# Kernel tuning notes

Hardware: AMD Instinct MI355X
Metric: run time of the kernel (lower is better)

The kernel has to match this reference:

```python
import jax, jax.numpy as jnp
import numpy as np

NUM_CATEGORIES = 10
FEATURE_DIM = 256
TEMPERATURE = 0.07
BATCH = 131072


def _l2norm(x, axis=-1, eps=1e-12):
    # matches torch F.normalize: x / max(||x||, eps)
    n = jnp.sqrt(jnp.sum(x * x, axis=axis, keepdims=True))
    return x / jnp.maximum(n, eps)


def setup_inputs() -> dict:
    key = jax.random.key(0)
    k1, k2, k3 = jax.random.split(key, 3)
    features = jax.random.normal(k1, (BATCH, FEATURE_DIM), dtype=jnp.float32)
    category_ids = jax.random.randint(k2, (BATCH,), 0, NUM_CATEGORIES, dtype=jnp.int32)
    # learned prototypes parameter, row-normalized at init as in the module
    prototypes = _l2norm(jax.random.normal(k3, (NUM_CATEGORIES, FEATURE_DIM), dtype=jnp.float32), axis=1)
    return {"features": features, "category_ids": category_ids, "prototypes": prototypes}


def reference(features, category_ids, prototypes):
    f = _l2norm(features, axis=1)  # [B, D]

    # per-category masked mean (segment mean), EMA prototype update (no_grad in torch)
    sums = jax.ops.segment_sum(f, category_ids, num_segments=NUM_CATEGORIES)  # [C, D]
    counts = jax.ops.segment_sum(jnp.ones((f.shape[0],), f.dtype), category_ids,
                                 num_segments=NUM_CATEGORIES)  # [C]
    means = sums / jnp.maximum(counts, 1.0)[:, None]
    ema = _l2norm(0.9 * prototypes + 0.1 * means, axis=1)
    updated = jnp.where((counts > 0)[:, None], ema, prototypes)  # [C, D]
    # torch writes into prototypes.data: value changes, param stays the autograd leaf
    p_used = prototypes + jax.lax.stop_gradient(updated - prototypes)

    # contrastive loss: one-hot cross entropy over categories
    sim = (f @ p_used.T) / TEMPERATURE  # [B, C]
    logp = jax.nn.log_softmax(sim, axis=1)
    b = f.shape[0]
    loss = -jnp.mean(logp[jnp.arange(b), category_ids])

    # align each feature with its category prototype
    aligned = _l2norm(0.7 * f + 0.3 * p_used[category_ids], axis=1)  # [B, D]
    return (loss, aligned)
```

## Files before the change

### kernel.cpp

```cpp
#include <hip/hip_runtime.h>

#define B_TOTAL 131072
#define DIM 256
#define NCAT 10

#define K1_BLOCKS 1024
#define K1_WAVES  (K1_BLOCKS * 4)
#define K3_BLOCKS 1024
#define NPART 16
#define SLABS_PER_PART (K1_BLOCKS / NPART)

#define SCR_STRIDE 2576
#define WS_SCRATCH 0
#define WS_PART2   (K1_BLOCKS * SCR_STRIDE)
#define WS_PUSED   (WS_PART2 + NCAT * NPART * 272)
#define WS_K3PART  (WS_PUSED + NCAT * DIM)

typedef __attribute__((ext_vector_type(8))) short bf16x8;
typedef __attribute__((ext_vector_type(4))) float f32x4;

union Frag { bf16x8 v; unsigned u[4]; };

__device__ __forceinline__ float waveRedSum(float v) {
#pragma unroll
  for (int m = 1; m < 64; m <<= 1) v += __shfl_xor(v, m, 64);
  return v;
}

__device__ __forceinline__ unsigned pk2(float a, float b) {
  unsigned ua = __float_as_uint(a), ub = __float_as_uint(b);
  ua = (ua + 0x7fffu + ((ua >> 16) & 1u)) >> 16;
  ub = (ub + 0x7fffu + ((ub >> 16) & 1u)) >> 16;
  return ua | (ub << 16);
}

__global__ __launch_bounds__(256) void k1_segsum(
    const float* __restrict__ feats, const int* __restrict__ cats,
    float* __restrict__ scratch) {
  __shared__ float acc[4][NCAT * DIM];
  __shared__ float accCnt[4][16];

  const int tid = threadIdx.x;
  const int w = tid >> 6;
  const int lane = tid & 63;

  for (int i = tid; i < 4 * NCAT * DIM; i += 256) (&acc[0][0])[i] = 0.0f;
  __syncthreads();

  float* accW = acc[w];
  int cnt = 0;
  int qd = blockIdx.x * 4 + w;

  const float* fp = feats + (size_t)qd * 4 * DIM + lane * 4;
  float4 A0 = *(const float4*)(fp);
  float4 A1 = *(const float4*)(fp + DIM);
  float4 A2 = *(const float4*)(fp + 2 * DIM);
  float4 A3 = *(const float4*)(fp + 3 * DIM);
  int c0 = cats[4 * qd], c1 = cats[4 * qd + 1];
  int c2 = cats[4 * qd + 2], c3 = cats[4 * qd + 3];

  for (int it = 0; it < 8; ++it) {
    const int qn = qd + K1_WAVES;
    float4 B0, B1, B2, B3;
    int d0 = 0, d1 = 0, d2 = 0, d3 = 0;
    if (it < 7) {
      const float* fn = feats + (size_t)qn * 4 * DIM + lane * 4;
      B0 = *(const float4*)(fn);
      B1 = *(const float4*)(fn + DIM);
      B2 = *(const float4*)(fn + 2 * DIM);
      B3 = *(const float4*)(fn + 3 * DIM);
      d0 = cats[4 * qn]; d1 = cats[4 * qn + 1];
      d2 = cats[4 * qn + 2]; d3 = cats[4 * qn + 3];
    }

    float s0 = A0.x * A0.x + A0.y * A0.y + A0.z * A0.z + A0.w * A0.w;
    float s1 = A1.x * A1.x + A1.y * A1.y + A1.z * A1.z + A1.w * A1.w;
    float s2 = A2.x * A2.x + A2.y * A2.y + A2.z * A2.z + A2.w * A2.w;
    float s3 = A3.x * A3.x + A3.y * A3.y + A3.z * A3.z + A3.w * A3.w;
#pragma unroll
    for (int m = 1; m < 64; m <<= 1) {
      s0 += __shfl_xor(s0, m, 64);
      s1 += __shfl_xor(s1, m, 64);
      s2 += __shfl_xor(s2, m, 64);
      s3 += __shfl_xor(s3, m, 64);
    }
    const float i0 = __builtin_amdgcn_rsqf(fmaxf(s0, 1e-24f));
    const float i1 = __builtin_amdgcn_rsqf(fmaxf(s1, 1e-24f));
    const float i2 = __builtin_amdgcn_rsqf(fmaxf(s2, 1e-24f));
    const float i3 = __builtin_amdgcn_rsqf(fmaxf(s3, 1e-24f));

    float4* p;
    float4 t;
    p = (float4*)&accW[c0 * DIM + lane * 4]; t = *p;
    t.x += A0.x * i0; t.y += A0.y * i0; t.z += A0.z * i0; t.w += A0.w * i0; *p = t;
    p = (float4*)&accW[c1 * DIM + lane * 4]; t = *p;
    t.x += A1.x * i1; t.y += A1.y * i1; t.z += A1.z * i1; t.w += A1.w * i1; *p = t;
    p = (float4*)&accW[c2 * DIM + lane * 4]; t = *p;
    t.x += A2.x * i2; t.y += A2.y * i2; t.z += A2.z * i2; t.w += A2.w * i2; *p = t;
    p = (float4*)&accW[c3 * DIM + lane * 4]; t = *p;
    t.x += A3.x * i3; t.y += A3.y * i3; t.z += A3.z * i3; t.w += A3.w * i3; *p = t;

    cnt += (lane == c0) + (lane == c1) + (lane == c2) + (lane == c3);

    if (it < 7) {
      A0 = B0; A1 = B1; A2 = B2; A3 = B3;
      c0 = d0; c1 = d1; c2 = d2; c3 = d3;
      qd = qn;
    }
  }

  if (lane < 16) accCnt[w][lane] = (float)cnt;
  __syncthreads();

  float* dst = scratch + (size_t)blockIdx.x * SCR_STRIDE;
  for (int i = tid; i < NCAT * DIM; i += 256)
    dst[i] = acc[0][i] + acc[1][i] + acc[2][i] + acc[3][i];
  if (tid < 16)
    dst[2560 + tid] = accCnt[0][tid] + accCnt[1][tid]
                    + accCnt[2][tid] + accCnt[3][tid];
}

__global__ __launch_bounds__(256) void k2a_reduce(
    const float* __restrict__ scratch, float* __restrict__ part) {
  const int b = blockIdx.x;
  const int c = b >> 4, p = b & 15;
  const int d = threadIdx.x;

  const float* base = scratch + (size_t)p * SLABS_PER_PART * SCR_STRIDE + c * DIM + d;
  float s0 = 0.f, s1 = 0.f, s2 = 0.f, s3 = 0.f;
#pragma unroll 4
  for (int s = 0; s < SLABS_PER_PART; s += 4) {
    s0 += base[(size_t)s * SCR_STRIDE];
    s1 += base[(size_t)(s + 1) * SCR_STRIDE];
    s2 += base[(size_t)(s + 2) * SCR_STRIDE];
    s3 += base[(size_t)(s + 3) * SCR_STRIDE];
  }
  part[b * 272 + d] = (s0 + s1) + (s2 + s3);

  if (d < 64) {
    float cn = scratch[((size_t)p * SLABS_PER_PART + d) * SCR_STRIDE + 2560 + c];
    cn = waveRedSum(cn);
    if (d == 0) part[b * 272 + 256] = cn;
  }
}

__global__ __launch_bounds__(256) void k2b_ema(
    const float* __restrict__ protos, const float* __restrict__ part,
    float* __restrict__ pused) {
  __shared__ float red[4];
  const int c = blockIdx.x;
  const int d = threadIdx.x;
  const int w = d >> 6, lane = d & 63;

  float s = 0.f, cnt = 0.f;
#pragma unroll
  for (int p = 0; p < NPART; p++) {
    s += part[(c * NPART + p) * 272 + d];
    cnt += part[(c * NPART + p) * 272 + 256];
  }

  const float pv = protos[c * DIM + d];
  const float v = 0.9f * pv + 0.1f * (s / fmaxf(cnt, 1.0f));

  float vv = waveRedSum(v * v);
  if (lane == 0) red[w] = vv;
  __syncthreads();
  const float n = fmaxf(sqrtf(red[0] + red[1] + red[2] + red[3]), 1e-12f);

  pused[c * DIM + d] = (cnt > 0.0f) ? v / n : pv;
}

__global__ __launch_bounds__(256) void k3_main(
    const float* __restrict__ feats, const int* __restrict__ cats,
    const float* __restrict__ pused, float* __restrict__ out,
    float* __restrict__ partials) {
  __shared__ unsigned short ot[4][16 * 272];
  __shared__ float wloss[4];

  const int tid = threadIdx.x;
  const int w = tid >> 6;
  const int l = tid & 63;
  const int q = l >> 4;
  const int mr = l & 15;
  char* otb = (char*)&ot[w][0];

  Frag bfr[8];
  {
    const float* prow = pused + mr * DIM;
#pragma unroll
    for (int s = 0; s < 8; s++) {
      float4 b0 = make_float4(0.f, 0.f, 0.f, 0.f), b1 = b0;
      const int kb = q * 8 + 32 * s;
      if (mr < NCAT) {
        b0 = *(const float4*)(prow + kb);
        b1 = *(const float4*)(prow + kb + 4);
      }
      bfr[s].u[0] = pk2(b0.x, b0.y); bfr[s].u[1] = pk2(b0.z, b0.w);
      bfr[s].u[2] = pk2(b1.x, b1.y); bfr[s].u[3] = pk2(b1.z, b1.w);
    }
  }

  constexpr float KZ = (1.0f / 0.07f) * 1.44269504088896f;
  constexpr float LN2 = 0.69314718056f;
  float lossAcc = 0.0f;

  const int waveG = blockIdx.x * 4 + w;
  const int nwaves = K3_BLOCKS * 4;

  for (int t = waveG; t < B_TOTAL / 16; t += nwaves) {
    const int r0 = t * 16;

    const float* frow = feats + (size_t)(r0 + mr) * DIM;
    Frag afr[8];
    float ss = 0.0f;
#pragma unroll
    for (int s = 0; s < 8; s++) {
      const int kb = q * 8 + 32 * s;
      const float4 u0 = *(const float4*)(frow + kb);
      const float4 u1 = *(const float4*)(frow + kb + 4);
      ss += u0.x * u0.x + u0.y * u0.y + u0.z * u0.z + u0.w * u0.w
          + u1.x * u1.x + u1.y * u1.y + u1.z * u1.z + u1.w * u1.w;
      afr[s].u[0] = pk2(u0.x, u0.y); afr[s].u[1] = pk2(u0.z, u0.w);
      afr[s].u[2] = pk2(u1.x, u1.y); afr[s].u[3] = pk2(u1.z, u1.w);
    }
    ss += __shfl_xor(ss, 16, 64);
    ss += __shfl_xor(ss, 32, 64);
    const float inv = __builtin_amdgcn_rsqf(fmaxf(ss, 1e-24f));

    f32x4 acc = {0.f, 0.f, 0.f, 0.f};
#pragma unroll
    for (int s = 0; s < 8; s++)
      acc = __builtin_amdgcn_mfma_f32_16x16x32_bf16(afr[s].v, bfr[s].v, acc, 0, 0, 0);

    float stv[4];
#pragma unroll
    for (int j = 0; j < 4; j++) {
      const float invj = __shfl(inv, 4 * q + j, 64);
      const int catj = cats[r0 + 4 * q + j];
      const float z = acc[j] * (invj * KZ);
      float zm = (mr < NCAT) ? z : -3.0e38f;
#pragma unroll
      for (int m = 1; m < 16; m <<= 1) zm = fmaxf(zm, __shfl_xor(zm, m, 64));
      float e = (mr < NCAT) ? __builtin_amdgcn_exp2f(z - zm) : 0.0f;
      float sv = (mr == catj) ? z : 0.0f;
#pragma unroll
      for (int m = 1; m < 16; m <<= 1) {
        e += __shfl_xor(e, m, 64);
        sv += __shfl_xor(sv, m, 64);
      }
      lossAcc += LN2 * (zm + __builtin_amdgcn_logf(e) - sv);
      stv[j] = sv;
    }

    const int srcg = (mr >> 2) * 16;
    const float s0 = __shfl(stv[0], srcg, 64);
    const float s1 = __shfl(stv[1], srcg, 64);
    const float s2 = __shfl(stv[2], srcg, 64);
    const float s3 = __shfl(stv[3], srcg, 64);
    const int jj = mr & 3;
    const float stm = (jj == 0) ? s0 : ((jj == 1) ? s1 : ((jj == 2) ? s2 : s3));
    const float simn = stm * (0.07f * LN2);
    const float inv2 = __builtin_amdgcn_rsqf(fmaxf(0.58f + 0.42f * simn, 1e-24f));
    const int catm = cats[r0 + mr];
    const float c0 = 0.7f * inv;
    const int psrc = q * 16 + catm;
    const int wrb = mr * 544;
    const int wsz = (mr & 7) << 4;

#pragma unroll
    for (int s = 0; s < 8; s++) {
      const int kb = q * 8 + 32 * s;
      unsigned pw0 = __shfl((int)bfr[s].u[0], psrc, 64);
      unsigned pw1 = __shfl((int)bfr[s].u[1], psrc, 64);
      unsigned pw2 = __shfl((int)bfr[s].u[2], psrc, 64);
      unsigned pw3 = __shfl((int)bfr[s].u[3], psrc, 64);
      const unsigned pws[4] = {pw0, pw1, pw2, pw3};
      float av[8];
#pragma unroll
      for (int h = 0; h < 4; h++) {
        const unsigned fp = afr[s].u[h];
        const unsigned pp = pws[h];
        const float f0 = __uint_as_float(fp << 16);
        const float f1 = __uint_as_float(fp & 0xffff0000u);
        const float p0 = __uint_as_float(pp << 16);
        const float p1 = __uint_as_float(pp & 0xffff0000u);
        av[2 * h]     = (c0 * f0 + 0.3f * p0) * inv2;
        av[2 * h + 1] = (c0 * f1 + 0.3f * p1) * inv2;
      }
      uint4 pk;
      pk.x = pk2(av[0], av[1]); pk.y = pk2(av[2], av[3]);
      pk.z = pk2(av[4], av[5]); pk.w = pk2(av[6], av[7]);
      *(uint4*)(otb + ((wrb + 2 * kb) ^ wsz)) = pk;
    }

    float* outr = out + (size_t)r0 * DIM;
#pragma unroll
    for (int i = 0; i < 16; ++i) {
      if (i == 15 && l == 63) continue;
      const int kidx = i * 64 + l + 1;
      const int rb = 544 * i;
      const int sz = (i & 7) << 4;
      const int cb = 8 * l + 6;
      float v[4];
#pragma unroll
      for (int c = 0; c < 4; ++c) {
        int a = (rb + cb + 2 * c) ^ sz;
        if (c > 0 && l == 63)
          a = (544 * (i + 1) + 2 * (c - 1)) ^ (((i + 1) & 7) << 4);
        v[c] = __uint_as_float((unsigned)(*(const unsigned short*)(otb + a)) << 16);
      }
      f32x4 sv = {v[0], v[1], v[2], v[3]};
      __builtin_nontemporal_store(sv, (f32x4*)(outr + 4 * kidx));
    }
    if (l < 3) {
      const float ev = __uint_as_float(
          (unsigned)(*(const unsigned short*)(otb + 2 * l)) << 16);
      __builtin_nontemporal_store(ev, outr + 1 + l);
    }
    if (l == 3) {
      const float ev = __uint_as_float(
          (unsigned)(*(const unsigned short*)(otb + ((544 * 15 + 510) ^ 112))) << 16);
      __builtin_nontemporal_store(ev, outr + 4096);
    }
  }

  const float s = waveRedSum(lossAcc);
  if (l == 0) wloss[w] = s * 0.0625f;
  __syncthreads();
  if (tid == 0)
    partials[blockIdx.x] = wloss[0] + wloss[1] + wloss[2] + wloss[3];
}

__global__ __launch_bounds__(256) void k4_loss(
    const float* __restrict__ partials, float* __restrict__ out) {
  __shared__ float red[4];
  const int tid = threadIdx.x;
  const int w = tid >> 6;
  const int lane = tid & 63;
  float s = 0.0f;
  for (int i = tid; i < K3_BLOCKS; i += 256) s += partials[i];
  s = waveRedSum(s);
  if (lane == 0) red[w] = s;
  __syncthreads();
  if (tid == 0)
    out[0] = (red[0] + red[1] + red[2] + red[3]) * (1.0f / (float)B_TOTAL);
}

extern "C" void kernel_launch(void* const* d_in, const int* in_sizes, int n_in,
                              void* d_out, int out_size, void* d_ws, size_t ws_size,
                              hipStream_t stream) {
  const float* feats = (const float*)d_in[0];
  const int* cats = (const int*)d_in[1];
  const float* protos = (const float*)d_in[2];
  float* out = (float*)d_out;
  float* ws = (float*)d_ws;

  k1_segsum<<<K1_BLOCKS, 256, 0, stream>>>(feats, cats, ws + WS_SCRATCH);
  k2a_reduce<<<NCAT * NPART, 256, 0, stream>>>(ws + WS_SCRATCH, ws + WS_PART2);
  k2b_ema<<<NCAT, 256, 0, stream>>>(protos, ws + WS_PART2, ws + WS_PUSED);
  k3_main<<<K3_BLOCKS, 256, 0, stream>>>(feats, cats, ws + WS_PUSED, out, ws + WS_K3PART);
  k4_loss<<<1, 256, 0, stream>>>(ws + WS_K3PART, out);
}
```

Before: 89.11 us.

## Cache normalized bf16 features from segsum pass and reuse in main kernel

The first kernel now writes the L2-normalized features as packed bf16 to workspace (64 MB fp32 read becomes a 32 MB bf16 write there). The main kernel then reads this half-size buffer instead of re-reading fp32 features and recomputing norms. The first kernel's feature loads are also made nontemporal. Net traffic changes from two 128 MB fp32 reads to one fp32 read plus a 64 MB bf16 write and a 64 MB bf16 read, and it adds 64 MB of workspace.

```diff
diff --git a/kernel.cpp b/kernel.cpp
--- a/kernel.cpp
+++ b/kernel.cpp
@@ -10,14 +10,16 @@
 #define NPART 16
 #define SLABS_PER_PART (K1_BLOCKS / NPART)
 
+#define WS_FHAT    0
+#define WS_SCRATCH (B_TOTAL * (DIM / 2))
 #define SCR_STRIDE 2576
-#define WS_SCRATCH 0
-#define WS_PART2   (K1_BLOCKS * SCR_STRIDE)
+#define WS_PART2   (WS_SCRATCH + K1_BLOCKS * SCR_STRIDE)
 #define WS_PUSED   (WS_PART2 + NCAT * NPART * 272)
 #define WS_K3PART  (WS_PUSED + NCAT * DIM)
 
 typedef __attribute__((ext_vector_type(8))) short bf16x8;
 typedef __attribute__((ext_vector_type(4))) float f32x4;
+typedef __attribute__((ext_vector_type(2))) unsigned u32x2;
 
 union Frag { bf16x8 v; unsigned u[4]; };
 
@@ -36,7 +38,7 @@
 
 __global__ __launch_bounds__(256) void k1_segsum(
     const float* __restrict__ feats, const int* __restrict__ cats,
-    float* __restrict__ scratch) {
+    unsigned* __restrict__ fhat, float* __restrict__ scratch) {
   __shared__ float acc[4][NCAT * DIM];
   __shared__ float accCnt[4][16];
 
@@ -51,24 +53,23 @@
   int cnt = 0;
   int qd = blockIdx.x * 4 + w;
 
-  const float* fp = feats + (size_t)qd * 4 * DIM + lane * 4;
-  float4 A0 = *(const float4*)(fp);
-  float4 A1 = *(const float4*)(fp + DIM);
-  float4 A2 = *(const float4*)(fp + 2 * DIM);
-  float4 A3 = *(const float4*)(fp + 3 * DIM);
+  const f32x4* fb = (const f32x4*)feats;
+  f32x4 A0 = __builtin_nontemporal_load(fb + (size_t)(4 * qd)     * 64 + lane);
+  f32x4 A1 = __builtin_nontemporal_load(fb + (size_t)(4 * qd + 1) * 64 + lane);
+  f32x4 A2 = __builtin_nontemporal_load(fb + (size_t)(4 * qd + 2) * 64 + lane);
+  f32x4 A3 = __builtin_nontemporal_load(fb + (size_t)(4 * qd + 3) * 64 + lane);
   int c0 = cats[4 * qd], c1 = cats[4 * qd + 1];
   int c2 = cats[4 * qd + 2], c3 = cats[4 * qd + 3];
 
   for (int it = 0; it < 8; ++it) {
     const int qn = qd + K1_WAVES;
-    float4 B0, B1, B2, B3;
+    f32x4 B0, B1, B2, B3;
     int d0 = 0, d1 = 0, d2 = 0, d3 = 0;
     if (it < 7) {
-      const float* fn = feats + (size_t)qn * 4 * DIM + lane * 4;
-      B0 = *(const float4*)(fn);
-      B1 = *(const float4*)(fn + DIM);
-      B2 = *(const float4*)(fn + 2 * DIM);
-      B3 = *(const float4*)(fn + 3 * DIM);
+      B0 = __builtin_nontemporal_load(fb + (size_t)(4 * qn)     * 64 + lane);
+      B1 = __builtin_nontemporal_load(fb + (size_t)(4 * qn + 1) * 64 + lane);
+      B2 = __builtin_nontemporal_load(fb + (size_t)(4 * qn + 2) * 64 + lane);
+      B3 = __builtin_nontemporal_load(fb + (size_t)(4 * qn + 3) * 64 + lane);
       d0 = cats[4 * qn]; d1 = cats[4 * qn + 1];
       d2 = cats[4 * qn + 2]; d3 = cats[4 * qn + 3];
     }
@@ -88,6 +89,16 @@
     const float i1 = __builtin_amdgcn_rsqf(fmaxf(s1, 1e-24f));
     const float i2 = __builtin_amdgcn_rsqf(fmaxf(s2, 1e-24f));
     const float i3 = __builtin_amdgcn_rsqf(fmaxf(s3, 1e-24f));
+
+    u32x2 h;
+    h.x = pk2(A0.x * i0, A0.y * i0); h.y = pk2(A0.z * i0, A0.w * i0);
+    *(u32x2*)(fhat + (size_t)(4 * qd)     * 128 + lane * 2) = h;
+    h.x = pk2(A1.x * i1, A1.y * i1); h.y = pk2(A1.z * i1, A1.w * i1);
+    *(u32x2*)(fhat + (size_t)(4 * qd + 1) * 128 + lane * 2) = h;
+    h.x = pk2(A2.x * i2, A2.y * i2); h.y = pk2(A2.z * i2, A2.w * i2);
+    *(u32x2*)(fhat + (size_t)(4 * qd + 2) * 128 + lane * 2) = h;
+    h.x = pk2(A3.x * i3, A3.y * i3); h.y = pk2(A3.z * i3, A3.w * i3);
+    *(u32x2*)(fhat + (size_t)(4 * qd + 3) * 128 + lane * 2) = h;
 
     float4* p;
     float4 t;
@@ -171,7 +182,7 @@
 }
 
 __global__ __launch_bounds__(256) void k3_main(
-    const float* __restrict__ feats, const int* __restrict__ cats,
+    const unsigned* __restrict__ fhat, const int* __restrict__ cats,
     const float* __restrict__ pused, float* __restrict__ out,
     float* __restrict__ partials) {
   __shared__ unsigned short ot[4][16 * 272];
@@ -210,22 +221,14 @@
   for (int t = waveG; t < B_TOTAL / 16; t += nwaves) {
     const int r0 = t * 16;
 
-    const float* frow = feats + (size_t)(r0 + mr) * DIM;
+    const uint4* fr = (const uint4*)(fhat + (size_t)(r0 + mr) * 128);
     Frag afr[8];
-    float ss = 0.0f;
 #pragma unroll
     for (int s = 0; s < 8; s++) {
-      const int kb = q * 8 + 32 * s;
-      const float4 u0 = *(const float4*)(frow + kb);
-      const float4 u1 = *(const float4*)(frow + kb + 4);
-      ss += u0.x * u0.x + u0.y * u0.y + u0.z * u0.z + u0.w * u0.w
-          + u1.x * u1.x + u1.y * u1.y + u1.z * u1.z + u1.w * u1.w;
-      afr[s].u[0] = pk2(u0.x, u0.y); afr[s].u[1] = pk2(u0.z, u0.w);
-      afr[s].u[2] = pk2(u1.x, u1.y); afr[s].u[3] = pk2(u1.z, u1.w);
-    }
-    ss += __shfl_xor(ss, 16, 64);
-    ss += __shfl_xor(ss, 32, 64);
-    const float inv = __builtin_amdgcn_rsqf(fmaxf(ss, 1e-24f));
+      const uint4 tt = fr[q + 4 * s];
+      afr[s].u[0] = tt.x; afr[s].u[1] = tt.y;
+      afr[s].u[2] = tt.z; afr[s].u[3] = tt.w;
+    }
 
     f32x4 acc = {0.f, 0.f, 0.f, 0.f};
 #pragma unroll
@@ -235,9 +238,8 @@
     float stv[4];
 #pragma unroll
     for (int j = 0; j < 4; j++) {
-      const float invj = __shfl(inv, 4 * q + j, 64);
       const int catj = cats[r0 + 4 * q + j];
-      const float z = acc[j] * (invj * KZ);
+      const float z = acc[j] * KZ;
       float zm = (mr < NCAT) ? z : -3.0e38f;
 #pragma unroll
       for (int m = 1; m < 16; m <<= 1) zm = fmaxf(zm, __shfl_xor(zm, m, 64));
@@ -262,7 +264,6 @@
     const float simn = stm * (0.07f * LN2);
     const float inv2 = __builtin_amdgcn_rsqf(fmaxf(0.58f + 0.42f * simn, 1e-24f));
     const int catm = cats[r0 + mr];
-    const float c0 = 0.7f * inv;
     const int psrc = q * 16 + catm;
     const int wrb = mr * 544;
     const int wsz = (mr & 7) << 4;
@@ -284,8 +285,8 @@
         const float f1 = __uint_as_float(fp & 0xffff0000u);
         const float p0 = __uint_as_float(pp << 16);
         const float p1 = __uint_as_float(pp & 0xffff0000u);
-        av[2 * h]     = (c0 * f0 + 0.3f * p0) * inv2;
-        av[2 * h + 1] = (c0 * f1 + 0.3f * p1) * inv2;
+        av[2 * h]     = (0.7f * f0 + 0.3f * p0) * inv2;
+        av[2 * h + 1] = (0.7f * f1 + 0.3f * p1) * inv2;
       }
       uint4 pk;
       pk.x = pk2(av[0], av[1]); pk.y = pk2(av[2], av[3]);
@@ -354,10 +355,11 @@
   const float* protos = (const float*)d_in[2];
   float* out = (float*)d_out;
   float* ws = (float*)d_ws;
-
-  k1_segsum<<<K1_BLOCKS, 256, 0, stream>>>(feats, cats, ws + WS_SCRATCH);
+  unsigned* fhat = (unsigned*)d_ws;
+
+  k1_segsum<<<K1_BLOCKS, 256, 0, stream>>>(feats, cats, fhat, ws + WS_SCRATCH);
   k2a_reduce<<<NCAT * NPART, 256, 0, stream>>>(ws + WS_SCRATCH, ws + WS_PART2);
   k2b_ema<<<NCAT, 256, 0, stream>>>(protos, ws + WS_PART2, ws + WS_PUSED);
-  k3_main<<<K3_BLOCKS, 256, 0, stream>>>(feats, cats, ws + WS_PUSED, out, ws + WS_K3PART);
+  k3_main<<<K3_BLOCKS, 256, 0, stream>>>(fhat, cats, ws + WS_PUSED, out, ws + WS_K3PART);
   k4_loss<<<1, 256, 0, stream>>>(ws + WS_K3PART, out);
 }
```

New measurement: 92.11 us. 1.03x slower.

## Fuse all stages into one cooperative kernel with bf16 normalized-feature cache

Applied to the files above, without the earlier changes.

Replaces the five-kernel chain with a single cooperative kernel of 512 blocks that uses grid.sync between the segment-sum, partial-reduce, EMA, main loss/align, and final-reduce phases. The first phase writes L2-normalized features as bf16 to workspace, so the main phase reads half the bytes and skips recomputing norms. Counts are now recomputed from category ids in the reduce phase. The change removes launch gaps and the second fp32 feature read, at the cost of grid-wide barriers, an extra bf16 write plus read of the features, and reduced parallelism. It falls back to the old multi-kernel path if cooperative launch is unavailable.

```diff
diff --git a/kernel.cpp b/kernel.cpp
--- a/kernel.cpp
+++ b/kernel.cpp
@@ -1,23 +1,16 @@
 #include <hip/hip_runtime.h>
+#include <hip/hip_cooperative_groups.h>
+
+namespace cg = cooperative_groups;
 
 #define B_TOTAL 131072
 #define DIM 256
 #define NCAT 10
-
-#define K1_BLOCKS 1024
-#define K1_WAVES  (K1_BLOCKS * 4)
-#define K3_BLOCKS 1024
 #define NPART 16
-#define SLABS_PER_PART (K1_BLOCKS / NPART)
-
-#define SCR_STRIDE 2576
-#define WS_SCRATCH 0
-#define WS_PART2   (K1_BLOCKS * SCR_STRIDE)
-#define WS_PUSED   (WS_PART2 + NCAT * NPART * 272)
-#define WS_K3PART  (WS_PUSED + NCAT * DIM)
 
 typedef __attribute__((ext_vector_type(8))) short bf16x8;
 typedef __attribute__((ext_vector_type(4))) float f32x4;
+typedef __attribute__((ext_vector_type(2))) unsigned u32x2;
 
 union Frag { bf16x8 v; unsigned u[4]; };
 
@@ -34,7 +27,329 @@
   return ua | (ub << 16);
 }
 
-__global__ __launch_bounds__(256) void k1_segsum(
+#define C_NB 512
+#define C_NWAVES (C_NB * 4)
+#define C_NQ (B_TOTAL / 4)
+#define C_SPP (C_NB / NPART)
+
+#define C_FHAT   0
+#define C_SCR    (B_TOTAL * (DIM / 2))
+#define C_PART   (C_SCR + C_NB * 2560)
+#define C_PUSED  (C_PART + NCAT * NPART * 272)
+#define C_LOSSP  (C_PUSED + NCAT * DIM)
+
+__global__ __launch_bounds__(256, 2) void kfused(
+    const float* __restrict__ feats, const int* __restrict__ cats,
+    const float* __restrict__ protos, float* __restrict__ out,
+    float* ws) {
+  __shared__ union {
+    float acc[4][NCAT * DIM];
+    struct { unsigned short ot[4][16 * 272]; float wloss[4]; } d;
+    float red[8];
+  } lds;
+
+  unsigned* fhat = (unsigned*)ws;
+  float* scratch = ws + C_SCR;
+  float* part = ws + C_PART;
+  float* pused = ws + C_PUSED;
+  float* lossp = ws + C_LOSSP;
+
+  const int tid = threadIdx.x;
+  const int blk = blockIdx.x;
+  const int w = tid >> 6;
+  const int lane = tid & 63;
+  cg::grid_group grid = cg::this_grid();
+
+  for (int i = tid; i < 4 * NCAT * DIM; i += 256) (&lds.acc[0][0])[i] = 0.0f;
+  __syncthreads();
+  {
+    float* accW = lds.acc[w];
+    const f32x4* fb = (const f32x4*)feats;
+    int qd = blk * 4 + w;
+
+    f32x4 A0 = fb[(size_t)(4 * qd)     * 64 + lane];
+    f32x4 A1 = fb[(size_t)(4 * qd + 1) * 64 + lane];
+    f32x4 A2 = fb[(size_t)(4 * qd + 2) * 64 + lane];
+    f32x4 A3 = fb[(size_t)(4 * qd + 3) * 64 + lane];
+    int c0 = cats[4 * qd], c1 = cats[4 * qd + 1];
+    int c2 = cats[4 * qd + 2], c3 = cats[4 * qd + 3];
+
+    for (;;) {
+      const int qn = qd + C_NWAVES;
+      const bool more = qn < C_NQ;
+      f32x4 B0, B1, B2, B3;
+      int d0 = 0, d1 = 0, d2 = 0, d3 = 0;
+      if (more) {
+        B0 = fb[(size_t)(4 * qn)     * 64 + lane];
+        B1 = fb[(size_t)(4 * qn + 1) * 64 + lane];
+        B2 = fb[(size_t)(4 * qn + 2) * 64 + lane];
+        B3 = fb[(size_t)(4 * qn + 3) * 64 + lane];
+        d0 = cats[4 * qn]; d1 = cats[4 * qn + 1];
+        d2 = cats[4 * qn + 2]; d3 = cats[4 * qn + 3];
+      }
+
+      float s0 = A0.x * A0.x + A0.y * A0.y + A0.z * A0.z + A0.w * A0.w;
+      float s1 = A1.x * A1.x + A1.y * A1.y + A1.z * A1.z + A1.w * A1.w;
+      float s2 = A2.x * A2.x + A2.y * A2.y + A2.z * A2.z + A2.w * A2.w;
+      float s3 = A3.x * A3.x + A3.y * A3.y + A3.z * A3.z + A3.w * A3.w;
+#pragma unroll
+      for (int m = 1; m < 64; m <<= 1) {
+        s0 += __shfl_xor(s0, m, 64);
+        s1 += __shfl_xor(s1, m, 64);
+        s2 += __shfl_xor(s2, m, 64);
+        s3 += __shfl_xor(s3, m, 64);
+      }
+      const float i0 = __builtin_amdgcn_rsqf(fmaxf(s0, 1e-24f));
+      const float i1 = __builtin_amdgcn_rsqf(fmaxf(s1, 1e-24f));
+      const float i2 = __builtin_amdgcn_rsqf(fmaxf(s2, 1e-24f));
+      const float i3 = __builtin_amdgcn_rsqf(fmaxf(s3, 1e-24f));
+
+      u32x2 h;
+      h.x = pk2(A0.x * i0, A0.y * i0); h.y = pk2(A0.z * i0, A0.w * i0);
+      *(u32x2*)(fhat + (size_t)(4 * qd)     * 128 + lane * 2) = h;
+      h.x = pk2(A1.x * i1, A1.y * i1); h.y = pk2(A1.z * i1, A1.w * i1);
+      *(u32x2*)(fhat + (size_t)(4 * qd + 1) * 128 + lane * 2) = h;
+      h.x = pk2(A2.x * i2, A2.y * i2); h.y = pk2(A2.z * i2, A2.w * i2);
+      *(u32x2*)(fhat + (size_t)(4 * qd + 2) * 128 + lane * 2) = h;
+      h.x = pk2(A3.x * i3, A3.y * i3); h.y = pk2(A3.z * i3, A3.w * i3);
+      *(u32x2*)(fhat + (size_t)(4 * qd + 3) * 128 + lane * 2) = h;
+
+      float4* p;
+      float4 t;
+      p = (float4*)&accW[c0 * DIM + lane * 4]; t = *p;
+      t.x += A0.x * i0; t.y += A0.y * i0; t.z += A0.z * i0; t.w += A0.w * i0; *p = t;
+      p = (float4*)&accW[c1 * DIM + lane * 4]; t = *p;
+      t.x += A1.x * i1; t.y += A1.y * i1; t.z += A1.z * i1; t.w += A1.w * i1; *p = t;
+      p = (float4*)&accW[c2 * DIM + lane * 4]; t = *p;
+      t.x += A2.x * i2; t.y += A2.y * i2; t.z += A2.z * i2; t.w += A2.w * i2; *p = t;
+      p = (float4*)&accW[c3 * DIM + lane * 4]; t = *p;
+      t.x += A3.x * i3; t.y += A3.y * i3; t.z += A3.z * i3; t.w += A3.w * i3; *p = t;
+
+      if (!more) break;
+      A0 = B0; A1 = B1; A2 = B2; A3 = B3;
+      c0 = d0; c1 = d1; c2 = d2; c3 = d3;
+      qd = qn;
+    }
+  }
+  __syncthreads();
+  {
+    float* dst = scratch + (size_t)blk * 2560;
+    for (int i = tid; i < NCAT * DIM; i += 256)
+      dst[i] = lds.acc[0][i] + lds.acc[1][i] + lds.acc[2][i] + lds.acc[3][i];
+  }
+  grid.sync();
+
+  if (blk < NCAT * NPART) {
+    const int c = blk >> 4, p = blk & 15;
+    const float* base = scratch + (size_t)p * C_SPP * 2560 + c * DIM + tid;
+    float s0 = 0.f, s1 = 0.f, s2 = 0.f, s3 = 0.f;
+#pragma unroll 4
+    for (int s = 0; s < C_SPP; s += 4) {
+      s0 += base[(size_t)s * 2560];
+      s1 += base[(size_t)(s + 1) * 2560];
+      s2 += base[(size_t)(s + 2) * 2560];
+      s3 += base[(size_t)(s + 3) * 2560];
+    }
+    part[blk * 272 + tid] = (s0 + s1) + (s2 + s3);
+
+    int cnt = 0;
+    const int* cs = cats + p * (B_TOTAL / NPART);
+    for (int i = tid; i < B_TOTAL / NPART; i += 256) cnt += (cs[i] == c);
+    const float fc = waveRedSum((float)cnt);
+    if (lane == 0) lds.red[w] = fc;
+    __syncthreads();
+    if (tid == 0)
+      part[blk * 272 + 256] = lds.red[0] + lds.red[1] + lds.red[2] + lds.red[3];
+  }
+  grid.sync();
+
+  if (blk < NCAT) {
+    const int c = blk;
+    float s = 0.f, cnt = 0.f;
+#pragma unroll
+    for (int p = 0; p < NPART; p++) {
+      s += part[(c * NPART + p) * 272 + tid];
+      cnt += part[(c * NPART + p) * 272 + 256];
+    }
+    const float pv = protos[c * DIM + tid];
+    const float v = 0.9f * pv + 0.1f * (s / fmaxf(cnt, 1.0f));
+    const float vv = waveRedSum(v * v);
+    __syncthreads();
+    if (lane == 0) lds.red[w] = vv;
+    __syncthreads();
+    const float n =
+        fmaxf(sqrtf(lds.red[0] + lds.red[1] + lds.red[2] + lds.red[3]), 1e-12f);
+    pused[c * DIM + tid] = (cnt > 0.0f) ? v / n : pv;
+  }
+  grid.sync();
+
+  {
+    const int l = lane;
+    const int q = l >> 4;
+    const int mr = l & 15;
+    char* otb = (char*)&lds.d.ot[w][0];
+
+    Frag bfr[8];
+    {
+      const float* prow = pused + mr * DIM;
+#pragma unroll
+      for (int s = 0; s < 8; s++) {
+        float4 b0 = make_float4(0.f, 0.f, 0.f, 0.f), b1 = b0;
+        const int kb = q * 8 + 32 * s;
+        if (mr < NCAT) {
+          b0 = *(const float4*)(prow + kb);
+          b1 = *(const float4*)(prow + kb + 4);
+        }
+        bfr[s].u[0] = pk2(b0.x, b0.y); bfr[s].u[1] = pk2(b0.z, b0.w);
+        bfr[s].u[2] = pk2(b1.x, b1.y); bfr[s].u[3] = pk2(b1.z, b1.w);
+      }
+    }
+
+    constexpr float KZ = (1.0f / 0.07f) * 1.44269504088896f;
+    constexpr float LN2 = 0.69314718056f;
+    float lossAcc = 0.0f;
+    const int waveG = blk * 4 + w;
+
+    for (int t = waveG; t < B_TOTAL / 16; t += C_NWAVES) {
+      const int r0 = t * 16;
+
+      const uint4* fr = (const uint4*)(fhat + (size_t)(r0 + mr) * 128);
+      Frag afr[8];
+#pragma unroll
+      for (int s = 0; s < 8; s++) {
+        const uint4 tt = fr[q + 4 * s];
+        afr[s].u[0] = tt.x; afr[s].u[1] = tt.y;
+        afr[s].u[2] = tt.z; afr[s].u[3] = tt.w;
+      }
+
+      f32x4 acc = {0.f, 0.f, 0.f, 0.f};
+#pragma unroll
+      for (int s = 0; s < 8; s++)
+        acc = __builtin_amdgcn_mfma_f32_16x16x32_bf16(afr[s].v, bfr[s].v, acc, 0, 0, 0);
+
+      float stv[4];
+#pragma unroll
+      for (int j = 0; j < 4; j++) {
+        const int catj = cats[r0 + 4 * q + j];
+        const float z = acc[j] * KZ;
+        float zm = (mr < NCAT) ? z : -3.0e38f;
+#pragma unroll
+        for (int m = 1; m < 16; m <<= 1) zm = fmaxf(zm, __shfl_xor(zm, m, 64));
+        float e = (mr < NCAT) ? __builtin_amdgcn_exp2f(z - zm) : 0.0f;
+        float sv = (mr == catj) ? z : 0.0f;
+#pragma unroll
+        for (int m = 1; m < 16; m <<= 1) {
+          e += __shfl_xor(e, m, 64);
+          sv += __shfl_xor(sv, m, 64);
+        }
+        lossAcc += LN2 * (zm + __builtin_amdgcn_logf(e) - sv);
+        stv[j] = sv;
+      }
+
+      const int srcg = (mr >> 2) * 16;
+      const float s0 = __shfl(stv[0], srcg, 64);
+      const float s1 = __shfl(stv[1], srcg, 64);
+      const float s2 = __shfl(stv[2], srcg, 64);
+      const float s3 = __shfl(stv[3], srcg, 64);
+      const int jj = mr & 3;
+      const float stm = (jj == 0) ? s0 : ((jj == 1) ? s1 : ((jj == 2) ? s2 : s3));
+      const float simn = stm * (0.07f * LN2);
+      const float inv2 = __builtin_amdgcn_rsqf(fmaxf(0.58f + 0.42f * simn, 1e-24f));
+      const int catm = cats[r0 + mr];
+      const int psrc = q * 16 + catm;
+      const int wrb = mr * 544;
+      const int wsz = (mr & 7) << 4;
+
+#pragma unroll
+      for (int s = 0; s < 8; s++) {
+        const int kb = q * 8 + 32 * s;
+        unsigned pw0 = __shfl((int)bfr[s].u[0], psrc, 64);
+        unsigned pw1 = __shfl((int)bfr[s].u[1], psrc, 64);
+        unsigned pw2 = __shfl((int)bfr[s].u[2], psrc, 64);
+        unsigned pw3 = __shfl((int)bfr[s].u[3], psrc, 64);
+        const unsigned pws[4] = {pw0, pw1, pw2, pw3};
+        float av[8];
+#pragma unroll
+        for (int h = 0; h < 4; h++) {
+          const unsigned fp = afr[s].u[h];
+          const unsigned pp = pws[h];
+          const float f0 = __uint_as_float(fp << 16);
+          const float f1 = __uint_as_float(fp & 0xffff0000u);
+          const float p0 = __uint_as_float(pp << 16);
+          const float p1 = __uint_as_float(pp & 0xffff0000u);
+          av[2 * h]     = (0.7f * f0 + 0.3f * p0) * inv2;
+          av[2 * h + 1] = (0.7f * f1 + 0.3f * p1) * inv2;
+        }
+        uint4 pk;
+        pk.x = pk2(av[0], av[1]); pk.y = pk2(av[2], av[3]);
+        pk.z = pk2(av[4], av[5]); pk.w = pk2(av[6], av[7]);
+        *(uint4*)(otb + ((wrb + 2 * kb) ^ wsz)) = pk;
+      }
+
+      float* outr = out + (size_t)r0 * DIM;
+#pragma unroll
+      for (int i = 0; i < 16; ++i) {
+        if (i == 15 && l == 63) continue;
+        const int kidx = i * 64 + l + 1;
+        const int rb = 544 * i;
+        const int sz = (i & 7) << 4;
+        const int cb = 8 * l + 6;
+        float v[4];
+#pragma unroll
+        for (int c = 0; c < 4; ++c) {
+          int a = (rb + cb + 2 * c) ^ sz;
+          if (c > 0 && l == 63)
+            a = (544 * (i + 1) + 2 * (c - 1)) ^ (((i + 1) & 7) << 4);
+          v[c] = __uint_as_float((unsigned)(*(const unsigned short*)(otb + a)) << 16);
+        }
+        f32x4 sv = {v[0], v[1], v[2], v[3]};
+        __builtin_nontemporal_store(sv, (f32x4*)(outr + 4 * kidx));
+      }
+      if (l < 3) {
+        const float ev = __uint_as_float(
+            (unsigned)(*(const unsigned short*)(otb + 2 * l)) << 16);
+        __builtin_nontemporal_store(ev, outr + 1 + l);
+      }
+      if (l == 3) {
+        const float ev = __uint_as_float(
+            (unsigned)(*(const unsigned short*)(otb + ((544 * 15 + 510) ^ 112))) << 16);
+        __builtin_nontemporal_store(ev, outr + 4096);
+      }
+    }
+
+    const float s = waveRedSum(lossAcc);
+    if (l == 0) lds.d.wloss[w] = s * 0.0625f;
+    __syncthreads();
+    if (tid == 0)
+      lossp[blk] = lds.d.wloss[0] + lds.d.wloss[1] + lds.d.wloss[2] + lds.d.wloss[3];
+  }
+  grid.sync();
+
+  if (blk == 0) {
+    float s = 0.f;
+    for (int i = tid; i < C_NB; i += 256) s += lossp[i];
+    s = waveRedSum(s);
+    __syncthreads();
+    if (lane == 0) lds.red[w] = s;
+    __syncthreads();
+    if (tid == 0)
+      out[0] = (lds.red[0] + lds.red[1] + lds.red[2] + lds.red[3]) *
+               (1.0f / (float)B_TOTAL);
+  }
+}
+
+#define F_K1_BLOCKS 1024
+#define F_K1_WAVES  (F_K1_BLOCKS * 4)
+#define F_K3_BLOCKS 1024
+#define F_SPP (F_K1_BLOCKS / NPART)
+
+#define F_SCR_STRIDE 2576
+#define F_SCRATCH 0
+#define F_PART2   (F_K1_BLOCKS * F_SCR_STRIDE)
+#define F_PUSED   (F_PART2 + NCAT * NPART * 272)
+#define F_K3PART  (F_PUSED + NCAT * DIM)
+
+__global__ __launch_bounds__(256) void fk1_segsum(
     const float* __restrict__ feats, const int* __restrict__ cats,
     float* __restrict__ scratch) {
   __shared__ float acc[4][NCAT * DIM];
@@ -60,7 +375,7 @@
   int c2 = cats[4 * qd + 2], c3 = cats[4 * qd + 3];
 
   for (int it = 0; it < 8; ++it) {
-    const int qn = qd + K1_WAVES;
+    const int qn = qd + F_K1_WAVES;
     float4 B0, B1, B2, B3;
     int d0 = 0, d1 = 0, d2 = 0, d3 = 0;
     if (it < 7) {
@@ -112,7 +427,7 @@
   if (lane < 16) accCnt[w][lane] = (float)cnt;
   __syncthreads();
 
-  float* dst = scratch + (size_t)blockIdx.x * SCR_STRIDE;
+  float* dst = scratch + (size_t)blockIdx.x * F_SCR_STRIDE;
   for (int i = tid; i < NCAT * DIM; i += 256)
     dst[i] = acc[0][i] + acc[1][i] + acc[2][i] + acc[3][i];
   if (tid < 16)
@@ -120,31 +435,31 @@
                     + accCnt[2][tid] + accCnt[3][tid];
 }
 
-__global__ __launch_bounds__(256) void k2a_reduce(
+__global__ __launch_bounds__(256) void fk2a_reduce(
     const float* __restrict__ scratch, float* __restrict__ part) {
   const int b = blockIdx.x;
   const int c = b >> 4, p = b & 15;
   const int d = threadIdx.x;
 
-  const float* base = scratch + (size_t)p * SLABS_PER_PART * SCR_STRIDE + c * DIM + d;
+  const float* base = scratch + (size_t)p * F_SPP * F_SCR_STRIDE + c * DIM + d;
   float s0 = 0.f, s1 = 0.f, s2 = 0.f, s3 = 0.f;
 #pragma unroll 4
-  for (int s = 0; s < SLABS_PER_PART; s += 4) {
-    s0 += base[(size_t)s * SCR_STRIDE];
-    s1 += base[(size_t)(s + 1) * SCR_STRIDE];
-    s2 += base[(size_t)(s + 2) * SCR_STRIDE];
-    s3 += base[(size_t)(s + 3) * SCR_STRIDE];
+  for (int s = 0; s < F_SPP; s += 4) {
+    s0 += base[(size_t)s * F_SCR_STRIDE];
+    s1 += base[(size_t)(s + 1) * F_SCR_STRIDE];
+    s2 += base[(size_t)(s + 2) * F_SCR_STRIDE];
+    s3 += base[(size_t)(s + 3) * F_SCR_STRIDE];
   }
   part[b * 272 + d] = (s0 + s1) + (s2 + s3);
 
   if (d < 64) {
-    float cn = scratch[((size_t)p * SLABS_PER_PART + d) * SCR_STRIDE + 2560 + c];
+    float cn = scratch[((size_t)p * F_SPP + d) * F_SCR_STRIDE + 2560 + c];
     cn = waveRedSum(cn);
     if (d == 0) part[b * 272 + 256] = cn;
   }
 }
 
-__global__ __launch_bounds__(256) void k2b_ema(
+__global__ __launch_bounds__(256) void fk2b_ema(
     const float* __restrict__ protos, const float* __restrict__ part,
     float* __restrict__ pused) {
   __shared__ float red[4];
@@ -170,7 +485,7 @@
   pused[c * DIM + d] = (cnt > 0.0f) ? v / n : pv;
 }
 
-__global__ __launch_bounds__(256) void k3_main(
+__global__ __launch_bounds__(256) void fk3_main(
     const float* __restrict__ feats, const int* __restrict__ cats,
     const float* __restrict__ pused, float* __restrict__ out,
     float* __restrict__ partials) {
@@ -205,7 +520,7 @@
   float lossAcc = 0.0f;
 
   const int waveG = blockIdx.x * 4 + w;
-  const int nwaves = K3_BLOCKS * 4;
+  const int nwaves = F_K3_BLOCKS * 4;
 
   for (int t = waveG; t < B_TOTAL / 16; t += nwaves) {
     const int r0 = t * 16;
@@ -262,7 +577,7 @@
     const float simn = stm * (0.07f * LN2);
     const float inv2 = __builtin_amdgcn_rsqf(fmaxf(0.58f + 0.42f * simn, 1e-24f));
     const int catm = cats[r0 + mr];
-    const float c0 = 0.7f * inv;
+    const float c0f = 0.7f * inv;
     const int psrc = q * 16 + catm;
     const int wrb = mr * 544;
     const int wsz = (mr & 7) << 4;
@@ -284,8 +599,8 @@
         const float f1 = __uint_as_float(fp & 0xffff0000u);
         const float p0 = __uint_as_float(pp << 16);
         const float p1 = __uint_as_float(pp & 0xffff0000u);
-        av[2 * h]     = (c0 * f0 + 0.3f * p0) * inv2;
-        av[2 * h + 1] = (c0 * f1 + 0.3f * p1) * inv2;
+        av[2 * h]     = (c0f * f0 + 0.3f * p0) * inv2;
+        av[2 * h + 1] = (c0f * f1 + 0.3f * p1) * inv2;
       }
       uint4 pk;
       pk.x = pk2(av[0], av[1]); pk.y = pk2(av[2], av[3]);
@@ -331,14 +646,14 @@
     partials[blockIdx.x] = wloss[0] + wloss[1] + wloss[2] + wloss[3];
 }
 
-__global__ __launch_bounds__(256) void k4_loss(
+__global__ __launch_bounds__(256) void fk4_loss(
     const float* __restrict__ partials, float* __restrict__ out) {
   __shared__ float red[4];
   const int tid = threadIdx.x;
   const int w = tid >> 6;
   const int lane = tid & 63;
   float s = 0.0f;
-  for (int i = tid; i < K3_BLOCKS; i += 256) s += partials[i];
+  for (int i = tid; i < F_K3_BLOCKS; i += 256) s += partials[i];
   s = waveRedSum(s);
   if (lane == 0) red[w] = s;
   __syncthreads();
@@ -355,9 +670,25 @@
   float* out = (float*)d_out;
   float* ws = (float*)d_ws;
 
-  k1_segsum<<<K1_BLOCKS, 256, 0, stream>>>(feats, cats, ws + WS_SCRATCH);
-  k2a_reduce<<<NCAT * NPART, 256, 0, stream>>>(ws + WS_SCRATCH, ws + WS_PART2);
-  k2b_ema<<<NCAT, 256, 0, stream>>>(protos, ws + WS_PART2, ws + WS_PUSED);
-  k3_main<<<K3_BLOCKS, 256, 0, stream>>>(feats, cats, ws + WS_PUSED, out, ws + WS_K3PART);
-  k4_loss<<<1, 256, 0, stream>>>(ws + WS_K3PART, out);
-}
+  int dev = 0;
+  hipGetDevice(&dev);
+  int coopAttr = 0;
+  hipDeviceGetAttribute(&coopAttr, hipDeviceAttributeCooperativeLaunch, dev);
+  int occ = 0;
+  hipError_t oe = hipOccupancyMaxActiveBlocksPerMultiprocessor(&occ, kfused, 256, 0);
+
+  if (coopAttr && oe == hipSuccess && occ >= 2) {
+    void* args[] = {(void*)&feats, (void*)&cats, (void*)&protos,
+                    (void*)&out, (void*)&ws};
+    hipError_t le = hipLaunchCooperativeKernel(kfused, dim3(C_NB), dim3(256),
+                                               args, 0, stream);
+    if (le == hipSuccess) return;
+  }
+
+  fk1_segsum<<<F_K1_BLOCKS, 256, 0, stream>>>(feats, cats, ws + F_SCRATCH);
+  fk2a_reduce<<<NCAT * NPART, 256, 0, stream>>>(ws + F_SCRATCH, ws + F_PART2);
+  fk2b_ema<<<NCAT, 256, 0, stream>>>(protos, ws + F_PART2, ws + F_PUSED);
+  fk3_main<<<F_K3_BLOCKS, 256, 0, stream>>>(feats, cats, ws + F_PUSED, out,
+                                            ws + F_K3PART);
+  fk4_loss<<<1, 256, 0, stream>>>(ws + F_K3PART, out);
+}
```

Result: no change. 89.47 us (+0.4%).

## Fuse EMA and loss-reduction kernels via last-block atomic counters, widen LDS reads

Applied to the files above, without the earlier changes.

Merges the small EMA-prototype kernel into the partial-reduce kernel and the final loss reduction into the main kernel. In each case the last block to finish, detected with an atomic counter and thread fences, does the tail work, which cuts the launch count from five to three. The counters are reset at the start of the first kernel. The output repack also swaps four 16-bit LDS reads for two 64-bit reads per lane. The costs are a serial tail in one block and atomic/fence overhead.

```diff
diff --git a/kernel.cpp b/kernel.cpp
--- a/kernel.cpp
+++ b/kernel.cpp
@@ -3,18 +3,19 @@
 #define B_TOTAL 131072
 #define DIM 256
 #define NCAT 10
+#define NPART 16
 
 #define K1_BLOCKS 1024
 #define K1_WAVES  (K1_BLOCKS * 4)
 #define K3_BLOCKS 1024
-#define NPART 16
-#define SLABS_PER_PART (K1_BLOCKS / NPART)
+#define SPP (K1_BLOCKS / NPART)
 
 #define SCR_STRIDE 2576
 #define WS_SCRATCH 0
-#define WS_PART2   (K1_BLOCKS * SCR_STRIDE)
-#define WS_PUSED   (WS_PART2 + NCAT * NPART * 272)
-#define WS_K3PART  (WS_PUSED + NCAT * DIM)
+#define WS_PART    (K1_BLOCKS * SCR_STRIDE)
+#define WS_PUSED   (WS_PART + NCAT * NPART * 272)
+#define WS_LOSSP   (WS_PUSED + NCAT * DIM)
+#define WS_CTR     (WS_LOSSP + K3_BLOCKS)
 
 typedef __attribute__((ext_vector_type(8))) short bf16x8;
 typedef __attribute__((ext_vector_type(4))) float f32x4;
@@ -36,13 +37,15 @@
 
 __global__ __launch_bounds__(256) void k1_segsum(
     const float* __restrict__ feats, const int* __restrict__ cats,
-    float* __restrict__ scratch) {
+    float* __restrict__ scratch, unsigned* __restrict__ ctrs) {
   __shared__ float acc[4][NCAT * DIM];
   __shared__ float accCnt[4][16];
 
   const int tid = threadIdx.x;
   const int w = tid >> 6;
   const int lane = tid & 63;
+
+  if (blockIdx.x == 0 && tid < 2) ctrs[tid] = 0u;
 
   for (int i = tid; i < 4 * NCAT * DIM; i += 256) (&acc[0][0])[i] = 0.0f;
   __syncthreads();
@@ -120,16 +123,21 @@
                     + accCnt[2][tid] + accCnt[3][tid];
 }
 
-__global__ __launch_bounds__(256) void k2a_reduce(
-    const float* __restrict__ scratch, float* __restrict__ part) {
+__global__ __launch_bounds__(256) void k2_fused(
+    const float* __restrict__ protos, const float* __restrict__ scratch,
+    float* __restrict__ part, float* __restrict__ pused,
+    unsigned* __restrict__ ctr) {
+  __shared__ float red[4];
+  __shared__ int lastFlag;
   const int b = blockIdx.x;
   const int c = b >> 4, p = b & 15;
   const int d = threadIdx.x;
-
-  const float* base = scratch + (size_t)p * SLABS_PER_PART * SCR_STRIDE + c * DIM + d;
+  const int w = d >> 6, lane = d & 63;
+
+  const float* base = scratch + (size_t)p * SPP * SCR_STRIDE + c * DIM + d;
   float s0 = 0.f, s1 = 0.f, s2 = 0.f, s3 = 0.f;
 #pragma unroll 4
-  for (int s = 0; s < SLABS_PER_PART; s += 4) {
+  for (int s = 0; s < SPP; s += 4) {
     s0 += base[(size_t)s * SCR_STRIDE];
     s1 += base[(size_t)(s + 1) * SCR_STRIDE];
     s2 += base[(size_t)(s + 2) * SCR_STRIDE];
@@ -138,44 +146,43 @@
   part[b * 272 + d] = (s0 + s1) + (s2 + s3);
 
   if (d < 64) {
-    float cn = scratch[((size_t)p * SLABS_PER_PART + d) * SCR_STRIDE + 2560 + c];
+    float cn = scratch[((size_t)p * SPP + d) * SCR_STRIDE + 2560 + c];
     cn = waveRedSum(cn);
     if (d == 0) part[b * 272 + 256] = cn;
   }
-}
-
-__global__ __launch_bounds__(256) void k2b_ema(
-    const float* __restrict__ protos, const float* __restrict__ part,
-    float* __restrict__ pused) {
-  __shared__ float red[4];
-  const int c = blockIdx.x;
-  const int d = threadIdx.x;
-  const int w = d >> 6, lane = d & 63;
-
-  float s = 0.f, cnt = 0.f;
-#pragma unroll
-  for (int p = 0; p < NPART; p++) {
-    s += part[(c * NPART + p) * 272 + d];
-    cnt += part[(c * NPART + p) * 272 + 256];
-  }
-
-  const float pv = protos[c * DIM + d];
-  const float v = 0.9f * pv + 0.1f * (s / fmaxf(cnt, 1.0f));
-
-  float vv = waveRedSum(v * v);
-  if (lane == 0) red[w] = vv;
-  __syncthreads();
-  const float n = fmaxf(sqrtf(red[0] + red[1] + red[2] + red[3]), 1e-12f);
-
-  pused[c * DIM + d] = (cnt > 0.0f) ? v / n : pv;
-}
-
-__global__ __launch_bounds__(256) void k3_main(
+
+  __threadfence();
+  __syncthreads();
+  if (d == 0) lastFlag = (atomicAdd(ctr, 1u) == NCAT * NPART - 1);
+  __syncthreads();
+  if (!lastFlag) return;
+  __threadfence();
+
+  for (int c2 = 0; c2 < NCAT; ++c2) {
+    float s = 0.f, cnt = 0.f;
+#pragma unroll
+    for (int p2 = 0; p2 < NPART; p2++) {
+      s += part[(c2 * NPART + p2) * 272 + d];
+      cnt += part[(c2 * NPART + p2) * 272 + 256];
+    }
+    const float pv = protos[c2 * DIM + d];
+    const float v = 0.9f * pv + 0.1f * (s / fmaxf(cnt, 1.0f));
+    const float vv = waveRedSum(v * v);
+    if (lane == 0) red[w] = vv;
+    __syncthreads();
+    const float n = fmaxf(sqrtf(red[0] + red[1] + red[2] + red[3]), 1e-12f);
+    pused[c2 * DIM + d] = (cnt > 0.0f) ? v / n : pv;
+    __syncthreads();
+  }
+}
+
+__global__ __launch_bounds__(256) void k3_fused(
     const float* __restrict__ feats, const int* __restrict__ cats,
     const float* __restrict__ pused, float* __restrict__ out,
-    float* __restrict__ partials) {
+    float* __restrict__ partials, unsigned* __restrict__ ctr) {
   __shared__ unsigned short ot[4][16 * 272];
   __shared__ float wloss[4];
+  __shared__ int lastFlag;
 
   const int tid = threadIdx.x;
   const int w = tid >> 6;
@@ -262,7 +269,7 @@
     const float simn = stm * (0.07f * LN2);
     const float inv2 = __builtin_amdgcn_rsqf(fmaxf(0.58f + 0.42f * simn, 1e-24f));
     const int catm = cats[r0 + mr];
-    const float c0 = 0.7f * inv;
+    const float c0f = 0.7f * inv;
     const int psrc = q * 16 + catm;
     const int wrb = mr * 544;
     const int wsz = (mr & 7) << 4;
@@ -284,8 +291,8 @@
         const float f1 = __uint_as_float(fp & 0xffff0000u);
         const float p0 = __uint_as_float(pp << 16);
         const float p1 = __uint_as_float(pp & 0xffff0000u);
-        av[2 * h]     = (c0 * f0 + 0.3f * p0) * inv2;
-        av[2 * h + 1] = (c0 * f1 + 0.3f * p1) * inv2;
+        av[2 * h]     = (c0f * f0 + 0.3f * p0) * inv2;
+        av[2 * h + 1] = (c0f * f1 + 0.3f * p1) * inv2;
       }
       uint4 pk;
       pk.x = pk2(av[0], av[1]); pk.y = pk2(av[2], av[3]);
@@ -300,16 +307,19 @@
       const int kidx = i * 64 + l + 1;
       const int rb = 544 * i;
       const int sz = (i & 7) << 4;
-      const int cb = 8 * l + 6;
-      float v[4];
-#pragma unroll
-      for (int c = 0; c < 4; ++c) {
-        int a = (rb + cb + 2 * c) ^ sz;
-        if (c > 0 && l == 63)
-          a = (544 * (i + 1) + 2 * (c - 1)) ^ (((i + 1) & 7) << 4);
-        v[c] = __uint_as_float((unsigned)(*(const unsigned short*)(otb + a)) << 16);
-      }
-      f32x4 sv = {v[0], v[1], v[2], v[3]};
+      const int aA = (rb + 8 * l) ^ sz;
+      const int aB = (l == 63) ? ((rb + 544) ^ (((i + 1) & 7) << 4))
+                               : ((rb + 8 * l + 8) ^ sz);
+      const unsigned long long A = *(const unsigned long long*)(otb + aA);
+      const unsigned long long Bv = *(const unsigned long long*)(otb + aB);
+      const unsigned a1 = (unsigned)(A >> 32);
+      const unsigned b0 = (unsigned)Bv;
+      const unsigned b1 = (unsigned)(Bv >> 32);
+      f32x4 sv;
+      sv.x = __uint_as_float(a1 & 0xffff0000u);
+      sv.y = __uint_as_float(b0 << 16);
+      sv.z = __uint_as_float(b0 & 0xffff0000u);
+      sv.w = __uint_as_float(b1 << 16);
       __builtin_nontemporal_store(sv, (f32x4*)(outr + 4 * kidx));
     }
     if (l < 3) {
@@ -327,23 +337,22 @@
   const float s = waveRedSum(lossAcc);
   if (l == 0) wloss[w] = s * 0.0625f;
   __syncthreads();
+  if (tid == 0) {
+    partials[blockIdx.x] = wloss[0] + wloss[1] + wloss[2] + wloss[3];
+    __threadfence();
+    lastFlag = (atomicAdd(ctr, 1u) == K3_BLOCKS - 1);
+  }
+  __syncthreads();
+  if (!lastFlag) return;
+  __threadfence();
+
+  float fs = 0.f;
+  for (int i = tid; i < K3_BLOCKS; i += 256) fs += partials[i];
+  fs = waveRedSum(fs);
+  if (l == 0) wloss[w] = fs;
+  __syncthreads();
   if (tid == 0)
-    partials[blockIdx.x] = wloss[0] + wloss[1] + wloss[2] + wloss[3];
-}
-
-__global__ __launch_bounds__(256) void k4_loss(
-    const float* __restrict__ partials, float* __restrict__ out) {
-  __shared__ float red[4];
-  const int tid = threadIdx.x;
-  const int w = tid >> 6;
-  const int lane = tid & 63;
-  float s = 0.0f;
-  for (int i = tid; i < K3_BLOCKS; i += 256) s += partials[i];
-  s = waveRedSum(s);
-  if (lane == 0) red[w] = s;
-  __syncthreads();
-  if (tid == 0)
-    out[0] = (red[0] + red[1] + red[2] + red[3]) * (1.0f / (float)B_TOTAL);
+    out[0] = (wloss[0] + wloss[1] + wloss[2] + wloss[3]) * (1.0f / (float)B_TOTAL);
 }
 
 extern "C" void kernel_launch(void* const* d_in, const int* in_sizes, int n_in,
@@ -354,10 +363,12 @@
   const float* protos = (const float*)d_in[2];
   float* out = (float*)d_out;
   float* ws = (float*)d_ws;
-
-  k1_segsum<<<K1_BLOCKS, 256, 0, stream>>>(feats, cats, ws + WS_SCRATCH);
-  k2a_reduce<<<NCAT * NPART, 256, 0, stream>>>(ws + WS_SCRATCH, ws + WS_PART2);
-  k2b_ema<<<NCAT, 256, 0, stream>>>(protos, ws + WS_PART2, ws + WS_PUSED);
-  k3_main<<<K3_BLOCKS, 256, 0, stream>>>(feats, cats, ws + WS_PUSED, out, ws + WS_K3PART);
-  k4_loss<<<1, 256, 0, stream>>>(ws + WS_K3PART, out);
-}
+  unsigned* ctrs = (unsigned*)(ws + WS_CTR);
+
+  k1_segsum<<<K1_BLOCKS, 256, 0, stream>>>(feats, cats, ws + WS_SCRATCH, ctrs);
+  k2_fused<<<NCAT * NPART, 256, 0, stream>>>(protos, ws + WS_SCRATCH,
+                                             ws + WS_PART, ws + WS_PUSED,
+                                             ctrs + 0);
+  k3_fused<<<K3_BLOCKS, 256, 0, stream>>>(feats, cats, ws + WS_PUSED, out,
+                                          ws + WS_LOSSP, ctrs + 1);
+}
```

Measured after the change: 150.8 us. +69.2%, slower.
